# Kernel optimization log

Measured on AMD Instinct MI355X. Metric: run time of the kernel, lower is better.

The kernel has to match this reference:

```python
import jax, jax.numpy as jnp
import numpy as np
from jax import lax

RANK = 4
N_ITERS = 20  # fixed ALS iteration count (tensorly default caps at 100 with tol; fixed count for jit)
EPS = 1e-6


def _khatri_rao(U, V):
    # column-wise Kronecker: (m, r) x (n, r) -> (m*n, r), row index i*n + j
    r = U.shape[1]
    return (U[:, None, :] * V[None, :, :]).reshape(-1, r)


def _cp_als_mode0(T, A, B, C):
    # CP-ALS on 3-way tensor T [I,J,K]; returns mode-0 factor A [I, r]
    I, J, K = T.shape
    T0 = T.reshape(I, J * K)                       # cols indexed j*K+k
    T1 = jnp.moveaxis(T, 1, 0).reshape(J, I * K)   # cols indexed i*K+k
    T2 = jnp.moveaxis(T, 2, 0).reshape(K, I * J)   # cols indexed i*J+j
    eye = EPS * jnp.eye(RANK, dtype=T.dtype)

    def step(carry, _):
        A, B, C = carry
        G = (B.T @ B) * (C.T @ C) + eye
        A = jnp.linalg.solve(G, (T0 @ _khatri_rao(B, C)).T).T
        G = (A.T @ A) * (C.T @ C) + eye
        B = jnp.linalg.solve(G, (T1 @ _khatri_rao(A, C)).T).T
        G = (A.T @ A) * (B.T @ B) + eye
        C = jnp.linalg.solve(G, (T2 @ _khatri_rao(A, B)).T).T
        return (A, B, C), None

    (A, B, C), _ = lax.scan(step, (A, B, C), None, length=N_ITERS)
    return A


def setup_inputs() -> dict:
    key = jax.random.key(0)
    ks = jax.random.split(key, 8)
    b, c, h, w = 256, 512, 14, 14
    red = 16
    x = jax.random.uniform(ks[0], (b, c, h, w), dtype=jnp.float32)
    # random ALS init factors (per sample)
    A0 = jax.random.uniform(ks[1], (b, c, RANK), dtype=jnp.float32)
    B0 = jax.random.uniform(ks[2], (b, h, RANK), dtype=jnp.float32)
    C0 = jax.random.uniform(ks[3], (b, w, RANK), dtype=jnp.float32)
    # rank_fc: Linear(rank,rank,bias=False), Linear(rank,1,bias=False)
    w1 = jax.random.normal(ks[4], (RANK, RANK), dtype=jnp.float32) / np.sqrt(RANK)
    w2 = jax.random.normal(ks[5], (1, RANK), dtype=jnp.float32) / np.sqrt(RANK)
    # fc: Linear(c, c//red), Linear(c//red, c)
    fw1 = jax.random.normal(ks[6], (c // red, c), dtype=jnp.float32) / np.sqrt(c)
    fw2 = jax.random.normal(ks[7], (c, c // red), dtype=jnp.float32) / np.sqrt(c // red)
    return {"x": x, "A0": A0, "B0": B0, "C0": C0, "w1": w1, "w2": w2, "fw1": fw1, "fw2": fw2}


def reference(x, A0, B0, C0, w1, w2, fw1, fw2):
    b, c, _, _ = x.shape
    # per-sample CP decomposition; keep channel-mode factor [b, c, rank]
    A = jax.vmap(_cp_als_mode0)(x, A0, B0, C0)
    # rank_fc: (b,c,rank) -> (b,c)
    y = jnp.maximum(jnp.einsum('bcr,sr->bcs', A, w1), 0.0)
    y = jnp.einsum('bcs,os->bco', y, w2)[..., 0]
    # SE fc: (b,c) -> sigmoid gate
    y = jnp.maximum(y @ fw1.T, 0.0)
    y = jax.nn.sigmoid(y @ fw2.T)
    return x * y[:, :, None, None]
```

## Files before the change

kernel.cpp:

```cpp
#include <hip/hip_runtime.h>


#define EPSV 1e-6f

#define SM_CTC  32
#define SM_ATA  104

typedef __attribute__((ext_vector_type(8))) short short8;
typedef __attribute__((ext_vector_type(4))) float float4v;

struct SMem {
  union {
    struct {
      short xhi[4 * 13 * 64 * 8];
      short xlo[4 * 13 * 64 * 8];
    } p1;
    struct {
      union {
        float gram[196 * 197];
        struct {
          short fh[7 * 64 * 8];
          short fl[7 * 64 * 8];
          float part[512 * 5];
        } f;
      } g;
      float H[196 * 5];
      float Y[196 * 5];
    } p2;
  } u;
  float B[56];
  float C[56];
  float Sm[120];
};

__device__ __forceinline__ float rlane(float v, int l) {
  return __uint_as_float(__builtin_amdgcn_readlane(__float_as_uint(v), l));
}
__device__ __forceinline__ void fence_lds() { __threadfence_block(); }

__device__ __forceinline__ unsigned bf16rne(float f) {
  unsigned u = __float_as_uint(f);
  return (u + 0x7FFFu + ((u >> 16) & 1u)) >> 16;
}

__device__ __forceinline__ float gram16(const float* V, int l) {
  int r = (l >> 2) & 3, s = l & 3;
  float a = 0.f;
#pragma unroll
  for (int j = 0; j < 14; ++j) a += V[j * 4 + r] * V[j * 4 + s];
  return a;
}

__device__ __forceinline__ float sel4(float a, float b, float c, float d, int k) {
  float x = (k & 1) ? b : a;
  float y = (k & 1) ? d : c;
  return (k & 2) ? y : x;
}

__device__ __forceinline__ void ginv_lanes(float myG, float gv[16]) {
  const float a00 = rlane(myG, 0),  a01 = rlane(myG, 1),  a02 = rlane(myG, 2),  a03 = rlane(myG, 3);
  const float a10 = rlane(myG, 4),  a11 = rlane(myG, 5),  a12 = rlane(myG, 6),  a13 = rlane(myG, 7);
  const float a20 = rlane(myG, 8),  a21 = rlane(myG, 9),  a22 = rlane(myG, 10), a23 = rlane(myG, 11);
  const float a30 = rlane(myG, 12), a31 = rlane(myG, 13), a32 = rlane(myG, 14), a33 = rlane(myG, 15);
  const float s0 = a00*a11 - a10*a01, s1 = a00*a12 - a10*a02, s2 = a00*a13 - a10*a03;
  const float s3 = a01*a12 - a11*a02, s4 = a01*a13 - a11*a03, s5 = a02*a13 - a12*a03;
  const float c5 = a22*a33 - a32*a23, c4 = a21*a33 - a31*a23, c3 = a21*a32 - a31*a22;
  const float c2 = a20*a33 - a30*a23, c1 = a20*a32 - a30*a22, c0 = a20*a31 - a30*a21;
  const float det = s0*c5 - s1*c4 + s2*c3 + s3*c2 - s4*c1 + s5*c0;
  const float rd = 1.0f / det;
  gv[0]  = ( a11*c5 - a12*c4 + a13*c3) * rd;
  gv[1]  = (-a01*c5 + a02*c4 - a03*c3) * rd;
  gv[2]  = ( a31*s5 - a32*s4 + a33*s3) * rd;
  gv[3]  = (-a21*s5 + a22*s4 - a23*s3) * rd;
  gv[4]  = (-a10*c5 + a12*c2 - a13*c1) * rd;
  gv[5]  = ( a00*c5 - a02*c2 + a03*c1) * rd;
  gv[6]  = (-a30*s5 + a32*s2 - a33*s1) * rd;
  gv[7]  = ( a20*s5 - a22*s2 + a23*s1) * rd;
  gv[8]  = ( a10*c4 - a11*c2 + a13*c0) * rd;
  gv[9]  = (-a00*c4 + a01*c2 - a03*c0) * rd;
  gv[10] = ( a30*s4 - a31*s2 + a33*s0) * rd;
  gv[11] = (-a20*s4 + a21*s2 - a23*s0) * rd;
  gv[12] = (-a10*c3 + a11*c1 - a12*c0) * rd;
  gv[13] = ( a00*c3 - a01*c1 + a02*c0) * rd;
  gv[14] = (-a30*s3 + a31*s1 - a32*s0) * rd;
  gv[15] = ( a20*s3 - a21*s1 + a22*s0) * rd;
}

__device__ __forceinline__ void computeH_scatter(SMem* sm, int l, const float gv[16],
                                                 bool scatter) {
#pragma unroll
  for (int k4 = 0; k4 < 4; ++k4) {
    int p = l + 64 * k4;
    if (p < 196) {
      int j = p / 14, kk = p - j * 14;
      float kr[4];
#pragma unroll
      for (int s = 0; s < 4; ++s) kr[s] = sm->B[j * 4 + s] * sm->C[kk * 4 + s];
      int kb = p >> 5, ii = p & 7, lrow = ((p >> 3) & 3) * 16;
#pragma unroll
      for (int r = 0; r < 4; ++r) {
        float h = kr[0] * gv[0 + r] + kr[1] * gv[4 + r]
                + kr[2] * gv[8 + r] + kr[3] * gv[12 + r];
        sm->u.p2.H[p * 5 + r] = h;
        if (scatter) {
          unsigned hh = bf16rne(h);
          float hf = __uint_as_float(hh << 16);
          unsigned ll = bf16rne(h - hf);
          int fi = (kb * 64 + lrow + r) * 8 + ii;
          sm->u.p2.g.f.fh[fi] = (short)hh;
          sm->u.p2.g.f.fl[fi] = (short)ll;
        }
      }
    }
  }
}

__device__ __forceinline__ void initial_H(SMem* sm, int l) {
  float btb = gram16(sm->B, l);
  float ctc = gram16(sm->C, l);
  float dgl = ((l >> 2) == (l & 3)) ? EPSV : 0.f;
  float myG = btb * ctc + dgl;
  float gv[16];
  ginv_lanes(myG, gv);
  if (l < 16) sm->Sm[SM_ATA + l] = 0.f;
  computeH_scatter(sm, l, gv, true);
}

__device__ __forceinline__ void factor_update(SMem* sm, int l, bool last) {
  const int jj = l >> 2, r = l & 3;
  const float dgl = ((l >> 2) == (l & 3)) ? EPSV : 0.f;
  const float ata = sm->Sm[SM_ATA + (l & 15)];
  const float ctc_old = sm->Sm[SM_CTC + (l & 15)];
  if (l < 16) sm->Sm[SM_ATA + l] = 0.f;
  float gv[16];
  float btb_new;
  {
    ginv_lanes(ata * ctc_old + dgl, gv);
    float m = 0.f;
    if (l < 56) {
#pragma unroll
      for (int k = 0; k < 14; ++k) m += sm->u.p2.Y[(jj * 14 + k) * 5 + r] * sm->C[k * 4 + r];
    }
    float bn = 0.f;
#pragma unroll
    for (int e = 0; e < 4; ++e) {
      float me = e ? __shfl_xor(m, e, 64) : m;
      float coef = sel4(gv[((0 ^ e) << 2) + 0], gv[((1 ^ e) << 2) + 1],
                        gv[((2 ^ e) << 2) + 2], gv[((3 ^ e) << 2) + 3], r);
      bn += me * coef;
    }
    if (l < 56) sm->B[l] = bn;
  }
  fence_lds();
  {
    btb_new = gram16(sm->B, l);
    ginv_lanes(ata * btb_new + dgl, gv);
    float m = 0.f;
    if (l < 56) {
#pragma unroll
      for (int j = 0; j < 14; ++j) m += sm->u.p2.Y[(j * 14 + jj) * 5 + r] * sm->B[j * 4 + r];
    }
    float cn = 0.f;
#pragma unroll
    for (int e = 0; e < 4; ++e) {
      float me = e ? __shfl_xor(m, e, 64) : m;
      float coef = sel4(gv[((0 ^ e) << 2) + 0], gv[((1 ^ e) << 2) + 1],
                        gv[((2 ^ e) << 2) + 2], gv[((3 ^ e) << 2) + 3], r);
      cn += me * coef;
    }
    if (l < 56) sm->C[l] = cn;
  }
  fence_lds();
  {
    float ctc_new = gram16(sm->C, l);
    ginv_lanes(btb_new * ctc_new + dgl, gv);
    computeH_scatter(sm, l, gv, !last);
  }
}

extern "C" __global__ void __launch_bounds__(1024, 4)
dese_kernel(const float* __restrict__ x, const float* __restrict__ B0,
            const float* __restrict__ C0, const float* __restrict__ w1,
            const float* __restrict__ w2, const float* __restrict__ fw1,
            const float* __restrict__ fw2, float* __restrict__ out) {
  extern __shared__ char smraw[];
  SMem* sm = (SMem*)smraw;
  const int tid = threadIdx.x;
  const int b = blockIdx.x;
  const int wv = tid >> 6;
  const int lane = tid & 63;
  const float* xb = x + (size_t)b * 100352;

  if (tid < 56) sm->B[tid] = B0[b * 56 + tid];
  if (tid >= 64 && tid < 120) sm->C[tid - 64] = C0[b * 56 + (tid - 64)];

  {
    const int R = (wv >= 4) + (wv >= 7) + (wv >= 10) + (wv >= 12) + (wv >= 14) + (wv >= 15);
    const int base = (R == 0) ? 0 : (R == 1) ? 4 : (R == 2) ? 7 : (R == 3) ? 10
                   : (R == 4) ? 12 : (R == 5) ? 14 : 15;
    const int I0 = 2 * R;
    const int J0 = I0 + 4 * (wv - base);
    const int IC1 = (I0 + 1 <= 12) ? I0 + 1 : 12;
    const bool iok1 = (I0 + 1 <= 12);

    int us_[4], upt_[4];
    bool uv_[4];
#pragma unroll
    for (int t = 0; t < 4; ++t) {
      int u = wv + 16 * t;
      uv_[t] = (u < 52);
      int s = uv_[t] ? (u / 13) : 0;
      us_[t] = s;
      upt_[t] = uv_[t] ? (u - s * 13) : 0;
    }
    const int pp_ = (lane & 15);
    const int co_ = (lane >> 4) * 8;

    float xr[4][8];
#define ISSUE_LOADS(CHUNK)                                                    \
    {                                                                         \
      _Pragma("unroll")                                                       \
      for (int t = 0; t < 4; ++t) {                                           \
        if (uv_[t]) {                                                         \
          int p = upt_[t] * 16 + pp_;                                         \
          int chb = (CHUNK) * 128 + us_[t] * 32 + co_;                        \
          _Pragma("unroll")                                                   \
          for (int ii = 0; ii < 8; ++ii)                                      \
            xr[t][ii] = (p < 196) ? xb[(size_t)(chb + ii) * 196 + p] : 0.f;   \
        }                                                                     \
      }                                                                       \
    }

    float4v acc0[4], acc1[4];
#pragma unroll
    for (int i = 0; i < 4; ++i) {
      acc0[i] = (float4v){0.f, 0.f, 0.f, 0.f};
      acc1[i] = (float4v){0.f, 0.f, 0.f, 0.f};
    }

    ISSUE_LOADS(0)
    for (int chunk = 0; chunk < 4; ++chunk) {
      __syncthreads();
#pragma unroll
      for (int t = 0; t < 4; ++t) {
        if (uv_[t]) {
          unsigned hp[4], lp[4];
#pragma unroll
          for (int ii = 0; ii < 8; ++ii) {
            float v = xr[t][ii];
            unsigned h = bf16rne(v);
            float hf = __uint_as_float(h << 16);
            unsigned lo2 = bf16rne(v - hf);
            if (ii & 1) { hp[ii >> 1] |= (h << 16); lp[ii >> 1] |= (lo2 << 16); }
            else        { hp[ii >> 1] = h;          lp[ii >> 1] = lo2; }
          }
          int fidx = (us_[t] * 13 + upt_[t]) * 64 + lane;
          *(uint4*)&sm->u.p1.xhi[fidx * 8] = make_uint4(hp[0], hp[1], hp[2], hp[3]);
          *(uint4*)&sm->u.p1.xlo[fidx * 8] = make_uint4(lp[0], lp[1], lp[2], lp[3]);
        }
      }
      __syncthreads();
      if (chunk < 3) ISSUE_LOADS(chunk + 1)
#pragma unroll
      for (int s = 0; s < 4; ++s) {
        const short8 aH0 = *(const short8*)&sm->u.p1.xhi[((s * 13 + I0)  * 64 + lane) * 8];
        const short8 aL0 = *(const short8*)&sm->u.p1.xlo[((s * 13 + I0)  * 64 + lane) * 8];
        const short8 aH1 = *(const short8*)&sm->u.p1.xhi[((s * 13 + IC1) * 64 + lane) * 8];
        const short8 aL1 = *(const short8*)&sm->u.p1.xlo[((s * 13 + IC1) * 64 + lane) * 8];
#pragma unroll
        for (int j = 0; j < 4; ++j) {
          const int J = J0 + j;
          if (J <= 12) {
            const short8 bH = *(const short8*)&sm->u.p1.xhi[((s * 13 + J) * 64 + lane) * 8];
            const short8 bL = *(const short8*)&sm->u.p1.xlo[((s * 13 + J) * 64 + lane) * 8];
            acc0[j] = __builtin_amdgcn_mfma_f32_16x16x32_bf16(aH0, bH, acc0[j], 0, 0, 0);
            acc0[j] = __builtin_amdgcn_mfma_f32_16x16x32_bf16(aH0, bL, acc0[j], 0, 0, 0);
            acc0[j] = __builtin_amdgcn_mfma_f32_16x16x32_bf16(aL0, bH, acc0[j], 0, 0, 0);
            if (iok1 && I0 + 1 <= J) {
              acc1[j] = __builtin_amdgcn_mfma_f32_16x16x32_bf16(aH1, bH, acc1[j], 0, 0, 0);
              acc1[j] = __builtin_amdgcn_mfma_f32_16x16x32_bf16(aH1, bL, acc1[j], 0, 0, 0);
              acc1[j] = __builtin_amdgcn_mfma_f32_16x16x32_bf16(aL1, bH, acc1[j], 0, 0, 0);
            }
          }
        }
      }
    }
#undef ISSUE_LOADS
    __syncthreads();
    {
      int col = lane & 15, quad = lane >> 4;
#define WRITE_TILE(ACC, I)                                          \
      {                                                             \
        int pc = (J0 + j) * 16 + col;                               \
        _Pragma("unroll")                                           \
        for (int reg = 0; reg < 4; ++reg) {                         \
          int pr = (I) * 16 + quad * 4 + reg;                       \
          if (pr < 196 && pc < 196) {                               \
            float v = ACC[j][reg];                                  \
            sm->u.p2.g.gram[pr * 197 + pc] = v;                     \
            sm->u.p2.g.gram[pc * 197 + pr] = v;                     \
          }                                                         \
        }                                                           \
      }
#pragma unroll
      for (int j = 0; j < 4; ++j) {
        const int J = J0 + j;
        if (J <= 12) {
          WRITE_TILE(acc0, I0)
          if (iok1 && I0 + 1 <= J) WRITE_TILE(acc1, I0 + 1)
        }
      }
#undef WRITE_TILE
    }
  }
  __syncthreads();

  short8 afh[7], afl[7];
  if (wv < 13) {
    const int m = wv * 16 + (lane & 15);
    const int mok = (m < 196);
    const int kq = (lane >> 4) * 8;
#pragma unroll
    for (int kb = 0; kb < 7; ++kb) {
#pragma unroll
      for (int i = 0; i < 8; ++i) {
        int k = kb * 32 + kq + i;
        float v = (mok && k < 196) ? sm->u.p2.g.gram[m * 197 + k] : 0.f;
        unsigned h = bf16rne(v);
        float hf = __uint_as_float(h << 16);
        unsigned lo = bf16rne(v - hf);
        afh[kb][i] = (short)h;
        afl[kb][i] = (short)lo;
      }
    }
  }
  __syncthreads();
  {
    unsigned* z = (unsigned*)sm->u.p2.g.f.fh;
#pragma unroll
    for (int t = 0; t < 4; ++t) {
      int idx = tid + 1024 * t;
      if (idx < 3584) z[idx] = 0u;
    }
  }
  __syncthreads();

  if (tid < 64) initial_H(sm, lane);
  __syncthreads();

  for (int it = 0; it < 19; ++it) {
    if (wv < 13) {
      float4v ac0 = {0.f, 0.f, 0.f, 0.f}, ac1 = {0.f, 0.f, 0.f, 0.f};
#pragma unroll
      for (int kb = 0; kb < 7; ++kb) {
        const short8 bh = *(const short8*)&sm->u.p2.g.f.fh[(kb * 64 + lane) * 8];
        const short8 bl = *(const short8*)&sm->u.p2.g.f.fl[(kb * 64 + lane) * 8];
        if (kb & 1) {
          ac1 = __builtin_amdgcn_mfma_f32_16x16x32_bf16(afh[kb], bh, ac1, 0, 0, 0);
          ac1 = __builtin_amdgcn_mfma_f32_16x16x32_bf16(afh[kb], bl, ac1, 0, 0, 0);
          ac1 = __builtin_amdgcn_mfma_f32_16x16x32_bf16(afl[kb], bh, ac1, 0, 0, 0);
        } else {
          ac0 = __builtin_amdgcn_mfma_f32_16x16x32_bf16(afh[kb], bh, ac0, 0, 0, 0);
          ac0 = __builtin_amdgcn_mfma_f32_16x16x32_bf16(afh[kb], bl, ac0, 0, 0, 0);
          ac0 = __builtin_amdgcn_mfma_f32_16x16x32_bf16(afl[kb], bh, ac0, 0, 0, 0);
        }
      }
      float4v acc = ac0 + ac1;
      const int col = lane & 15;
      const int quad = lane >> 4;
      const int row0 = wv * 16 + quad * 4;
      if (col < 4) {
#pragma unroll
        for (int reg = 0; reg < 4; ++reg) {
          int pr = row0 + reg;
          if (pr < 196) sm->u.p2.Y[pr * 5 + col] = acc[reg];
        }
        float pa0 = 0.f, pa1 = 0.f, pa2 = 0.f, pa3 = 0.f;
#pragma unroll
        for (int reg = 0; reg < 4; ++reg) {
          int pr = row0 + reg;
          if (pr < 196) {
            float yv = acc[reg];
            pa0 += sm->u.p2.H[pr * 5 + 0] * yv;
            pa1 += sm->u.p2.H[pr * 5 + 1] * yv;
            pa2 += sm->u.p2.H[pr * 5 + 2] * yv;
            pa3 += sm->u.p2.H[pr * 5 + 3] * yv;
          }
        }
        pa0 += __shfl_xor(pa0, 16, 64); pa0 += __shfl_xor(pa0, 32, 64);
        pa1 += __shfl_xor(pa1, 16, 64); pa1 += __shfl_xor(pa1, 32, 64);
        pa2 += __shfl_xor(pa2, 16, 64); pa2 += __shfl_xor(pa2, 32, 64);
        pa3 += __shfl_xor(pa3, 16, 64); pa3 += __shfl_xor(pa3, 32, 64);
        if (quad == 0) {
          atomicAdd(&sm->Sm[SM_ATA + 0 * 4 + col], pa0);
          atomicAdd(&sm->Sm[SM_ATA + 1 * 4 + col], pa1);
          atomicAdd(&sm->Sm[SM_ATA + 2 * 4 + col], pa2);
          atomicAdd(&sm->Sm[SM_ATA + 3 * 4 + col], pa3);
        }
      }
    } else if (wv == 13) {
      float ctc = gram16(sm->C, lane);
      if (lane < 16) sm->Sm[SM_CTC + lane] = ctc;
    }
    __syncthreads();
    if (tid < 64) factor_update(sm, lane, it == 18);
    __syncthreads();
  }

  {
    float hr[13];
#pragma unroll
    for (int k = 0; k < 13; ++k) {
      int d = 64 * k + lane;
      hr[k] = (d < 784) ? sm->u.p2.H[(d >> 2) * 5 + (d & 3)] : 0.f;
    }
    const int ch = tid & 511;
    const int half = tid >> 9;
    const float4* row = (const float4*)(xb + ch * 196);
    float a0 = 0.f, a1 = 0.f, a2 = 0.f, a3 = 0.f;
#define EPI_F4(F4)                                                     \
    {                                                                  \
      float4 v = row[(F4)];                                            \
      float vv[4] = {v.x, v.y, v.z, v.w};                              \
      _Pragma("unroll")                                                \
      for (int j = 0; j < 4; ++j) {                                    \
        int d = 16 * (F4) + 4 * j;                                     \
        a0 += vv[j] * rlane(hr[(d + 0) >> 6], (d + 0) & 63);           \
        a1 += vv[j] * rlane(hr[(d + 1) >> 6], (d + 1) & 63);           \
        a2 += vv[j] * rlane(hr[(d + 2) >> 6], (d + 2) & 63);           \
        a3 += vv[j] * rlane(hr[(d + 3) >> 6], (d + 3) & 63);           \
      }                                                                \
    }
    if (half == 0) {
#pragma unroll
      for (int f4 = 0; f4 < 25; ++f4) EPI_F4(f4)
    } else {
#pragma unroll
      for (int f4 = 25; f4 < 49; ++f4) EPI_F4(f4)
    }
#undef EPI_F4
    if (half) {
      float* pp = &sm->u.p2.g.f.part[ch * 5];
      pp[0] = a0; pp[1] = a1; pp[2] = a2; pp[3] = a3;
    }
    __syncthreads();
    if (tid < 512) {
      const float* pp = &sm->u.p2.g.f.part[tid * 5];
      a0 += pp[0]; a1 += pp[1]; a2 += pp[2]; a3 += pp[3];
      float y = 0.f;
#pragma unroll
      for (int s = 0; s < 4; ++s) {
        float pre = w1[s * 4 + 0] * a0 + w1[s * 4 + 1] * a1 + w1[s * 4 + 2] * a2
                  + w1[s * 4 + 3] * a3;
        y += w2[s] * fmaxf(pre, 0.f);
      }
      sm->u.p2.Y[tid] = y;
    }
  }
  __syncthreads();
  {
    int u = tid >> 5, lc = tid & 31;
    float a = 0.f;
#pragma unroll
    for (int k = 0; k < 16; ++k) {
      int c = lc + 32 * k;
      a += sm->u.p2.Y[c] * fw1[u * 512 + c];
    }
    a += __shfl_xor(a, 1, 64);
    a += __shfl_xor(a, 2, 64);
    a += __shfl_xor(a, 4, 64);
    a += __shfl_xor(a, 8, 64);
    a += __shfl_xor(a, 16, 64);
    if (lc == 0) sm->u.p2.Y[512 + u] = fmaxf(a, 0.f);
  }
  __syncthreads();
  if (tid < 512) {
    const float4* f2r = (const float4*)(fw2 + tid * 32);
    float za = 0.f;
#pragma unroll
    for (int u4 = 0; u4 < 8; ++u4) {
      float4 fv = f2r[u4];
      za += fv.x * sm->u.p2.Y[512 + u4 * 4 + 0];
      za += fv.y * sm->u.p2.Y[512 + u4 * 4 + 1];
      za += fv.z * sm->u.p2.Y[512 + u4 * 4 + 2];
      za += fv.w * sm->u.p2.Y[512 + u4 * 4 + 3];
    }
    float g = 1.f / (1.f + __expf(-za));
    sm->u.p2.Y[tid] = g;
  }
  __syncthreads();
  {
    const float4* xi = (const float4*)xb;
    float4* oo = (float4*)(out + (size_t)b * 100352);
#pragma unroll
    for (int t = 0; t < 25; ++t) {
      int v = tid + t * 1024;
      if (v < 25088) {
        float4 q = xi[v];
        float g = sm->u.p2.Y[v / 49];
        oo[v] = make_float4(q.x * g, q.y * g, q.z * g, q.w * g);
      }
    }
  }
}

extern "C" void kernel_launch(void* const* d_in, const int* in_sizes, int n_in,
                              void* d_out, int out_size, void* d_ws, size_t ws_size,
                              hipStream_t stream) {
  (void)in_sizes; (void)n_in; (void)d_ws; (void)ws_size; (void)out_size;
  const float* x   = (const float*)d_in[0];
  const float* B0  = (const float*)d_in[2];
  const float* C0  = (const float*)d_in[3];
  const float* w1  = (const float*)d_in[4];
  const float* w2  = (const float*)d_in[5];
  const float* fw1 = (const float*)d_in[6];
  const float* fw2 = (const float*)d_in[7];
  float* out = (float*)d_out;

  size_t shmem = sizeof(SMem);
  hipFuncSetAttribute((const void*)dese_kernel,
                      hipFuncAttributeMaxDynamicSharedMemorySize, (int)shmem);
  hipLaunchKernelGGL(dese_kernel, dim3(256), dim3(1024), shmem, stream,
                     x, B0, C0, w1, w2, fw1, fw2, out);
}
```

Before: 364.3 us.

## Double-buffer Gram staging, use hardware bf16 pack, compute Gram matrices in registers

The x-staging loop for the spatial Gram matrix now runs as 8 double-buffered chunks of 64 channels across 13 waves, replacing 4 single-buffered chunks of 128 channels. Conversion and store of the next chunk overlap with the MFMA work on the current one, which removes one barrier per chunk. The manual bf16 round-to-nearest-even code is replaced with the v_cvt_pk_bf16_f32 instruction throughout. In the ALS update, B^T B and C^T C are computed with register shuffles instead of LDS loops, and C^T C is passed between iterations in registers rather than computed by a separate wave. The costs are more loop iterations and barriers in the staging phase, and an inline-asm dependency on that instruction.

```diff
diff --git a/kernel.cpp b/kernel.cpp
--- a/kernel.cpp
+++ b/kernel.cpp
@@ -3,7 +3,6 @@
 
 #define EPSV 1e-6f
 
-#define SM_CTC  32
 #define SM_ATA  104
 
 typedef __attribute__((ext_vector_type(8))) short short8;
@@ -12,8 +11,8 @@
 struct SMem {
   union {
     struct {
-      short xhi[4 * 13 * 64 * 8];
-      short xlo[4 * 13 * 64 * 8];
+      short xhi[2 * 26 * 64 * 8];
+      short xlo[2 * 26 * 64 * 8];
     } p1;
     struct {
       union {
@@ -38,10 +37,12 @@
 }
 __device__ __forceinline__ void fence_lds() { __threadfence_block(); }
 
-__device__ __forceinline__ unsigned bf16rne(float f) {
-  unsigned u = __float_as_uint(f);
-  return (u + 0x7FFFu + ((u >> 16) & 1u)) >> 16;
-}
+__device__ __forceinline__ unsigned cvtpk(float a, float b) {
+  unsigned r;
+  asm("v_cvt_pk_bf16_f32 %0, %1, %2" : "=v"(r) : "v"(a), "v"(b));
+  return r;
+}
+__device__ __forceinline__ float asf(unsigned u) { return __uint_as_float(u); }
 
 __device__ __forceinline__ float gram16(const float* V, int l) {
   int r = (l >> 2) & 3, s = l & 3;
@@ -49,6 +50,25 @@
 #pragma unroll
   for (int j = 0; j < 14; ++j) a += V[j * 4 + r] * V[j * 4 + s];
   return a;
+}
+
+__device__ __forceinline__ float regGram(float v, int l) {
+  float S0 = v * v;
+  S0 += __shfl_xor(S0, 4, 64);  S0 += __shfl_xor(S0, 8, 64);
+  S0 += __shfl_xor(S0, 16, 64); S0 += __shfl_xor(S0, 32, 64);
+  float S1 = v * __shfl_xor(v, 1, 64);
+  S1 += __shfl_xor(S1, 4, 64);  S1 += __shfl_xor(S1, 8, 64);
+  S1 += __shfl_xor(S1, 16, 64); S1 += __shfl_xor(S1, 32, 64);
+  float S2 = v * __shfl_xor(v, 2, 64);
+  S2 += __shfl_xor(S2, 4, 64);  S2 += __shfl_xor(S2, 8, 64);
+  S2 += __shfl_xor(S2, 16, 64); S2 += __shfl_xor(S2, 32, 64);
+  float S3 = v * __shfl_xor(v, 3, 64);
+  S3 += __shfl_xor(S3, 4, 64);  S3 += __shfl_xor(S3, 8, 64);
+  S3 += __shfl_xor(S3, 16, 64); S3 += __shfl_xor(S3, 32, 64);
+  int e = ((l >> 2) ^ l) & 3;
+  float x = (e & 1) ? S1 : S0;
+  float y = (e & 1) ? S3 : S2;
+  return (e & 2) ? y : x;
 }
 
 __device__ __forceinline__ float sel4(float a, float b, float c, float d, int k) {
@@ -93,89 +113,89 @@
     int p = l + 64 * k4;
     if (p < 196) {
       int j = p / 14, kk = p - j * 14;
-      float kr[4];
-#pragma unroll
-      for (int s = 0; s < 4; ++s) kr[s] = sm->B[j * 4 + s] * sm->C[kk * 4 + s];
-      int kb = p >> 5, ii = p & 7, lrow = ((p >> 3) & 3) * 16;
-#pragma unroll
-      for (int r = 0; r < 4; ++r) {
-        float h = kr[0] * gv[0 + r] + kr[1] * gv[4 + r]
-                + kr[2] * gv[8 + r] + kr[3] * gv[12 + r];
-        sm->u.p2.H[p * 5 + r] = h;
-        if (scatter) {
-          unsigned hh = bf16rne(h);
-          float hf = __uint_as_float(hh << 16);
-          unsigned ll = bf16rne(h - hf);
-          int fi = (kb * 64 + lrow + r) * 8 + ii;
-          sm->u.p2.g.f.fh[fi] = (short)hh;
-          sm->u.p2.g.f.fl[fi] = (short)ll;
-        }
-      }
-    }
-  }
-}
-
-__device__ __forceinline__ void initial_H(SMem* sm, int l) {
+      float4 Bj = *(const float4*)&sm->B[j * 4];
+      float4 Ck = *(const float4*)&sm->C[kk * 4];
+      float kr0 = Bj.x * Ck.x, kr1 = Bj.y * Ck.y, kr2 = Bj.z * Ck.z, kr3 = Bj.w * Ck.w;
+      float h0 = kr0 * gv[0] + kr1 * gv[4] + kr2 * gv[8]  + kr3 * gv[12];
+      float h1 = kr0 * gv[1] + kr1 * gv[5] + kr2 * gv[9]  + kr3 * gv[13];
+      float h2 = kr0 * gv[2] + kr1 * gv[6] + kr2 * gv[10] + kr3 * gv[14];
+      float h3 = kr0 * gv[3] + kr1 * gv[7] + kr2 * gv[11] + kr3 * gv[15];
+      float* Hp = &sm->u.p2.H[p * 5];
+      Hp[0] = h0; Hp[1] = h1; Hp[2] = h2; Hp[3] = h3;
+      if (scatter) {
+        int fib = ((p >> 5) * 64 + ((p >> 3) & 3) * 16) * 8 + (p & 7);
+        unsigned pa = cvtpk(h0, h1), pb = cvtpk(h2, h3);
+        float la0 = h0 - asf(pa << 16), la1 = h1 - asf(pa & 0xFFFF0000u);
+        float lb0 = h2 - asf(pb << 16), lb1 = h3 - asf(pb & 0xFFFF0000u);
+        unsigned qa = cvtpk(la0, la1), qb = cvtpk(lb0, lb1);
+        short* fh = sm->u.p2.g.f.fh;
+        short* fl = sm->u.p2.g.f.fl;
+        fh[fib]      = (short)pa; fh[fib + 8]  = (short)(pa >> 16);
+        fh[fib + 16] = (short)pb; fh[fib + 24] = (short)(pb >> 16);
+        fl[fib]      = (short)qa; fl[fib + 8]  = (short)(qa >> 16);
+        fl[fib + 16] = (short)qb; fl[fib + 24] = (short)(qb >> 16);
+      }
+    }
+  }
+}
+
+__device__ __forceinline__ float initial_H(SMem* sm, int l) {
   float btb = gram16(sm->B, l);
   float ctc = gram16(sm->C, l);
   float dgl = ((l >> 2) == (l & 3)) ? EPSV : 0.f;
-  float myG = btb * ctc + dgl;
   float gv[16];
-  ginv_lanes(myG, gv);
+  ginv_lanes(btb * ctc + dgl, gv);
   if (l < 16) sm->Sm[SM_ATA + l] = 0.f;
   computeH_scatter(sm, l, gv, true);
-}
-
-__device__ __forceinline__ void factor_update(SMem* sm, int l, bool last) {
+  return ctc;
+}
+
+__device__ __forceinline__ float factor_update(SMem* sm, int l, float ctc_prev,
+                                               bool last) {
   const int jj = l >> 2, r = l & 3;
   const float dgl = ((l >> 2) == (l & 3)) ? EPSV : 0.f;
   const float ata = sm->Sm[SM_ATA + (l & 15)];
-  const float ctc_old = sm->Sm[SM_CTC + (l & 15)];
   if (l < 16) sm->Sm[SM_ATA + l] = 0.f;
   float gv[16];
-  float btb_new;
-  {
-    ginv_lanes(ata * ctc_old + dgl, gv);
-    float m = 0.f;
-    if (l < 56) {
-#pragma unroll
-      for (int k = 0; k < 14; ++k) m += sm->u.p2.Y[(jj * 14 + k) * 5 + r] * sm->C[k * 4 + r];
-    }
-    float bn = 0.f;
-#pragma unroll
-    for (int e = 0; e < 4; ++e) {
-      float me = e ? __shfl_xor(m, e, 64) : m;
-      float coef = sel4(gv[((0 ^ e) << 2) + 0], gv[((1 ^ e) << 2) + 1],
-                        gv[((2 ^ e) << 2) + 2], gv[((3 ^ e) << 2) + 3], r);
-      bn += me * coef;
-    }
-    if (l < 56) sm->B[l] = bn;
-  }
+  ginv_lanes(ata * ctc_prev + dgl, gv);
+  float m = 0.f;
+  if (l < 56) {
+#pragma unroll
+    for (int k = 0; k < 14; ++k) m += sm->u.p2.Y[(jj * 14 + k) * 5 + r] * sm->C[k * 4 + r];
+  }
+  float bn = 0.f;
+#pragma unroll
+  for (int e = 0; e < 4; ++e) {
+    float me = e ? __shfl_xor(m, e, 64) : m;
+    float coef = sel4(gv[((0 ^ e) << 2) + 0], gv[((1 ^ e) << 2) + 1],
+                      gv[((2 ^ e) << 2) + 2], gv[((3 ^ e) << 2) + 3], r);
+    bn += me * coef;
+  }
+  bn = (l < 56) ? bn : 0.f;
+  if (l < 56) sm->B[l] = bn;
   fence_lds();
-  {
-    btb_new = gram16(sm->B, l);
-    ginv_lanes(ata * btb_new + dgl, gv);
-    float m = 0.f;
-    if (l < 56) {
-#pragma unroll
-      for (int j = 0; j < 14; ++j) m += sm->u.p2.Y[(j * 14 + jj) * 5 + r] * sm->B[j * 4 + r];
-    }
-    float cn = 0.f;
-#pragma unroll
-    for (int e = 0; e < 4; ++e) {
-      float me = e ? __shfl_xor(m, e, 64) : m;
-      float coef = sel4(gv[((0 ^ e) << 2) + 0], gv[((1 ^ e) << 2) + 1],
-                        gv[((2 ^ e) << 2) + 2], gv[((3 ^ e) << 2) + 3], r);
-      cn += me * coef;
-    }
-    if (l < 56) sm->C[l] = cn;
-  }
+  const float btb_new = regGram(bn, l);
+  ginv_lanes(ata * btb_new + dgl, gv);
+  float m2 = 0.f;
+  if (l < 56) {
+#pragma unroll
+    for (int j = 0; j < 14; ++j) m2 += sm->u.p2.Y[(j * 14 + jj) * 5 + r] * sm->B[j * 4 + r];
+  }
+  float cn = 0.f;
+#pragma unroll
+  for (int e = 0; e < 4; ++e) {
+    float me = e ? __shfl_xor(m2, e, 64) : m2;
+    float coef = sel4(gv[((0 ^ e) << 2) + 0], gv[((1 ^ e) << 2) + 1],
+                      gv[((2 ^ e) << 2) + 2], gv[((3 ^ e) << 2) + 3], r);
+    cn += me * coef;
+  }
+  cn = (l < 56) ? cn : 0.f;
+  if (l < 56) sm->C[l] = cn;
   fence_lds();
-  {
-    float ctc_new = gram16(sm->C, l);
-    ginv_lanes(btb_new * ctc_new + dgl, gv);
-    computeH_scatter(sm, l, gv, !last);
-  }
+  const float ctc_new = regGram(cn, l);
+  ginv_lanes(btb_new * ctc_new + dgl, gv);
+  computeH_scatter(sm, l, gv, !last);
+  return ctc_new;
 }
 
 extern "C" __global__ void __launch_bounds__(1024, 4)
@@ -203,32 +223,37 @@
     const int IC1 = (I0 + 1 <= 12) ? I0 + 1 : 12;
     const bool iok1 = (I0 + 1 <= 12);
 
-    int us_[4], upt_[4];
-    bool uv_[4];
-#pragma unroll
-    for (int t = 0; t < 4; ++t) {
-      int u = wv + 16 * t;
-      uv_[t] = (u < 52);
-      int s = uv_[t] ? (u / 13) : 0;
-      us_[t] = s;
-      upt_[t] = uv_[t] ? (u - s * 13) : 0;
-    }
-    const int pp_ = (lane & 15);
+    const int pp_ = wv * 16 + (lane & 15);
     const int co_ = (lane >> 4) * 8;
-
-    float xr[4][8];
-#define ISSUE_LOADS(CHUNK)                                                    \
-    {                                                                         \
-      _Pragma("unroll")                                                       \
-      for (int t = 0; t < 4; ++t) {                                           \
-        if (uv_[t]) {                                                         \
-          int p = upt_[t] * 16 + pp_;                                         \
-          int chb = (CHUNK) * 128 + us_[t] * 32 + co_;                        \
-          _Pragma("unroll")                                                   \
-          for (int ii = 0; ii < 8; ++ii)                                      \
-            xr[t][ii] = (p < 196) ? xb[(size_t)(chb + ii) * 196 + p] : 0.f;   \
-        }                                                                     \
-      }                                                                       \
+    const bool stg = (wv < 13);
+
+    float xr[2][8];
+#define ISSUE_LOADS(CHUNK)                                                     \
+    {                                                                          \
+      _Pragma("unroll")                                                        \
+      for (int s2 = 0; s2 < 2; ++s2) {                                         \
+        int chb = (CHUNK) * 64 + s2 * 32 + co_;                                \
+        _Pragma("unroll")                                                      \
+        for (int ii = 0; ii < 8; ++ii)                                         \
+          xr[s2][ii] = (pp_ < 196) ? xb[(size_t)(chb + ii) * 196 + pp_] : 0.f; \
+      }                                                                        \
+    }
+#define CONVERT_STORE(BUF)                                                     \
+    {                                                                          \
+      _Pragma("unroll")                                                        \
+      for (int s2 = 0; s2 < 2; ++s2) {                                         \
+        unsigned hp[4], lp[4];                                                 \
+        _Pragma("unroll")                                                      \
+        for (int q = 0; q < 4; ++q) {                                          \
+          float v0 = xr[s2][2 * q], v1 = xr[s2][2 * q + 1];                    \
+          unsigned h = cvtpk(v0, v1);                                          \
+          float l0 = v0 - asf(h << 16), l1 = v1 - asf(h & 0xFFFF0000u);        \
+          hp[q] = h; lp[q] = cvtpk(l0, l1);                                    \
+        }                                                                      \
+        int fidx = (((BUF) * 26) + s2 * 13 + wv) * 64 + lane;                  \
+        *(uint4*)&sm->u.p1.xhi[fidx * 8] = make_uint4(hp[0], hp[1], hp[2], hp[3]); \
+        *(uint4*)&sm->u.p1.xlo[fidx * 8] = make_uint4(lp[0], lp[1], lp[2], lp[3]); \
+      }                                                                        \
     }
 
     float4v acc0[4], acc1[4];
@@ -238,41 +263,28 @@
       acc1[i] = (float4v){0.f, 0.f, 0.f, 0.f};
     }
 
-    ISSUE_LOADS(0)
-    for (int chunk = 0; chunk < 4; ++chunk) {
-      __syncthreads();
-#pragma unroll
-      for (int t = 0; t < 4; ++t) {
-        if (uv_[t]) {
-          unsigned hp[4], lp[4];
-#pragma unroll
-          for (int ii = 0; ii < 8; ++ii) {
-            float v = xr[t][ii];
-            unsigned h = bf16rne(v);
-            float hf = __uint_as_float(h << 16);
-            unsigned lo2 = bf16rne(v - hf);
-            if (ii & 1) { hp[ii >> 1] |= (h << 16); lp[ii >> 1] |= (lo2 << 16); }
-            else        { hp[ii >> 1] = h;          lp[ii >> 1] = lo2; }
-          }
-          int fidx = (us_[t] * 13 + upt_[t]) * 64 + lane;
-          *(uint4*)&sm->u.p1.xhi[fidx * 8] = make_uint4(hp[0], hp[1], hp[2], hp[3]);
-          *(uint4*)&sm->u.p1.xlo[fidx * 8] = make_uint4(lp[0], lp[1], lp[2], lp[3]);
-        }
-      }
-      __syncthreads();
-      if (chunk < 3) ISSUE_LOADS(chunk + 1)
-#pragma unroll
-      for (int s = 0; s < 4; ++s) {
-        const short8 aH0 = *(const short8*)&sm->u.p1.xhi[((s * 13 + I0)  * 64 + lane) * 8];
-        const short8 aL0 = *(const short8*)&sm->u.p1.xlo[((s * 13 + I0)  * 64 + lane) * 8];
-        const short8 aH1 = *(const short8*)&sm->u.p1.xhi[((s * 13 + IC1) * 64 + lane) * 8];
-        const short8 aL1 = *(const short8*)&sm->u.p1.xlo[((s * 13 + IC1) * 64 + lane) * 8];
+    if (stg) {
+      ISSUE_LOADS(0)
+      CONVERT_STORE(0)
+      ISSUE_LOADS(1)
+    }
+    __syncthreads();
+
+    for (int c = 0; c < 8; ++c) {
+      const int buf = c & 1;
+#pragma unroll
+      for (int s = 0; s < 2; ++s) {
+        const int ub = buf * 26 + s * 13;
+        const short8 aH0 = *(const short8*)&sm->u.p1.xhi[((ub + I0)  * 64 + lane) * 8];
+        const short8 aL0 = *(const short8*)&sm->u.p1.xlo[((ub + I0)  * 64 + lane) * 8];
+        const short8 aH1 = *(const short8*)&sm->u.p1.xhi[((ub + IC1) * 64 + lane) * 8];
+        const short8 aL1 = *(const short8*)&sm->u.p1.xlo[((ub + IC1) * 64 + lane) * 8];
 #pragma unroll
         for (int j = 0; j < 4; ++j) {
           const int J = J0 + j;
           if (J <= 12) {
-            const short8 bH = *(const short8*)&sm->u.p1.xhi[((s * 13 + J) * 64 + lane) * 8];
-            const short8 bL = *(const short8*)&sm->u.p1.xlo[((s * 13 + J) * 64 + lane) * 8];
+            const short8 bH = *(const short8*)&sm->u.p1.xhi[((ub + J) * 64 + lane) * 8];
+            const short8 bL = *(const short8*)&sm->u.p1.xlo[((ub + J) * 64 + lane) * 8];
             acc0[j] = __builtin_amdgcn_mfma_f32_16x16x32_bf16(aH0, bH, acc0[j], 0, 0, 0);
             acc0[j] = __builtin_amdgcn_mfma_f32_16x16x32_bf16(aH0, bL, acc0[j], 0, 0, 0);
             acc0[j] = __builtin_amdgcn_mfma_f32_16x16x32_bf16(aL0, bH, acc0[j], 0, 0, 0);
@@ -284,9 +296,12 @@
           }
         }
       }
+      if (stg && c + 1 < 8) CONVERT_STORE(buf ^ 1)
+      if (stg && c + 2 < 8) ISSUE_LOADS(c + 2)
+      __syncthreads();
     }
 #undef ISSUE_LOADS
-    __syncthreads();
+#undef CONVERT_STORE
     {
       int col = lane & 15, quad = lane >> 4;
 #define WRITE_TILE(ACC, I)                                          \
@@ -322,16 +337,20 @@
     const int kq = (lane >> 4) * 8;
 #pragma unroll
     for (int kb = 0; kb < 7; ++kb) {
-#pragma unroll
-      for (int i = 0; i < 8; ++i) {
-        int k = kb * 32 + kq + i;
-        float v = (mok && k < 196) ? sm->u.p2.g.gram[m * 197 + k] : 0.f;
-        unsigned h = bf16rne(v);
-        float hf = __uint_as_float(h << 16);
-        unsigned lo = bf16rne(v - hf);
-        afh[kb][i] = (short)h;
-        afl[kb][i] = (short)lo;
-      }
+      unsigned hw[4], lw[4];
+#pragma unroll
+      for (int q = 0; q < 4; ++q) {
+        int k0 = kb * 32 + kq + 2 * q;
+        float v0 = (mok && k0 < 196)     ? sm->u.p2.g.gram[m * 197 + k0]     : 0.f;
+        float v1 = (mok && k0 + 1 < 196) ? sm->u.p2.g.gram[m * 197 + k0 + 1] : 0.f;
+        unsigned h = cvtpk(v0, v1);
+        float l0 = v0 - asf(h << 16), l1 = v1 - asf(h & 0xFFFF0000u);
+        hw[q] = h; lw[q] = cvtpk(l0, l1);
+      }
+      uint4 th = make_uint4(hw[0], hw[1], hw[2], hw[3]);
+      uint4 tl = make_uint4(lw[0], lw[1], lw[2], lw[3]);
+      afh[kb] = *(short8*)&th;
+      afl[kb] = *(short8*)&tl;
     }
   }
   __syncthreads();
@@ -345,7 +364,8 @@
   }
   __syncthreads();
 
-  if (tid < 64) initial_H(sm, lane);
+  float ctc_prev = 0.f;
+  if (tid < 64) ctc_prev = initial_H(sm, lane);
   __syncthreads();
 
   for (int it = 0; it < 19; ++it) {
@@ -398,12 +418,9 @@
           atomicAdd(&sm->Sm[SM_ATA + 3 * 4 + col], pa3);
         }
       }
-    } else if (wv == 13) {
-      float ctc = gram16(sm->C, lane);
-      if (lane < 16) sm->Sm[SM_CTC + lane] = ctc;
     }
     __syncthreads();
-    if (tid < 64) factor_update(sm, lane, it == 18);
+    if (tid < 64) ctc_prev = factor_update(sm, lane, ctc_prev, it == 18);
     __syncthreads();
   }
 
```

New measurement: 308.2 us. -15.4%, faster.
